# Performance work log

Measured on AMD Instinct MI355X. Metric: run time of the kernel, lower is better.

Reference implementation:

```python
import jax, jax.numpy as jnp
import numpy as np

N = 50000
E = 800000
IN_CH = 128
HID = 128
HEADS = 8
OUT_CH = 40
NEG_SLOPE = 0.2
BN_EPS = 1e-5


def gat_conv(x, src, dst, W, a_src, a_dst, bias, heads, ch, concat):
    # x: [N, F_in]; W: [heads*ch, F_in]; a_src/a_dst: [heads, ch]; bias: [heads*ch] or [ch]
    n = x.shape[0]
    h = (x @ W.T).reshape(n, heads, ch)                      # [N, H, C]
    alpha_src = (h * a_src[None]).sum(-1)                    # [N, H]
    alpha_dst = (h * a_dst[None]).sum(-1)                    # [N, H]
    e = alpha_src[src] + alpha_dst[dst]                      # [E, H]
    e = jax.nn.leaky_relu(e, NEG_SLOPE)
    # segment softmax over incoming edges of each destination node
    emax = jax.ops.segment_max(e, dst, num_segments=n)       # [N, H]
    ee = jnp.exp(e - emax[dst])
    denom = jax.ops.segment_sum(ee, dst, num_segments=n)     # [N, H]
    alpha = ee / (denom[dst] + 1e-16)                        # [E, H]
    msg = h[src] * alpha[:, :, None]                         # [E, H, C]
    out = jax.ops.segment_sum(msg, dst, num_segments=n)      # [N, H, C]
    out = out.reshape(n, heads * ch) if concat else out.mean(axis=1)
    return out + bias


def batch_norm_eval(x, gamma, beta, mean, var):
    return (x - mean) * jax.lax.rsqrt(var + BN_EPS) * gamma + beta


def setup_inputs() -> dict:
    key = jax.random.key(0)
    ks = jax.random.split(key, 16)
    ch = HID // HEADS  # 16
    s = 1.0 / np.sqrt(IN_CH)
    inp = {
        "x": jax.random.normal(ks[0], (N, IN_CH), dtype=jnp.float32),
        "edge_index": jax.random.randint(ks[1], (2, E), 0, N, dtype=jnp.int64),
        # layer 0
        "W0": jax.random.normal(ks[2], (HEADS * ch, IN_CH), jnp.float32) * s,
        "a_src0": jax.random.normal(ks[3], (HEADS, ch), jnp.float32) * 0.1,
        "a_dst0": jax.random.normal(ks[4], (HEADS, ch), jnp.float32) * 0.1,
        "b0": jnp.zeros((HID,), jnp.float32),
        "bn_g0": jnp.ones((HID,), jnp.float32),
        "bn_b0": jnp.zeros((HID,), jnp.float32),
        "bn_m0": jnp.zeros((HID,), jnp.float32),
        "bn_v0": jnp.ones((HID,), jnp.float32),
        # layer 1
        "W1": jax.random.normal(ks[5], (HEADS * ch, HID), jnp.float32) * (1.0 / np.sqrt(HID)),
        "a_src1": jax.random.normal(ks[6], (HEADS, ch), jnp.float32) * 0.1,
        "a_dst1": jax.random.normal(ks[7], (HEADS, ch), jnp.float32) * 0.1,
        "b1": jnp.zeros((HID,), jnp.float32),
        "bn_g1": jnp.ones((HID,), jnp.float32),
        "bn_b1": jnp.zeros((HID,), jnp.float32),
        "bn_m1": jnp.zeros((HID,), jnp.float32),
        "bn_v1": jnp.ones((HID,), jnp.float32),
        # output layer (heads=1, concat=False)
        "W2": jax.random.normal(ks[8], (OUT_CH, HID), jnp.float32) * (1.0 / np.sqrt(HID)),
        "a_src2": jax.random.normal(ks[9], (1, OUT_CH), jnp.float32) * 0.1,
        "a_dst2": jax.random.normal(ks[10], (1, OUT_CH), jnp.float32) * 0.1,
        "b2": jnp.zeros((OUT_CH,), jnp.float32),
    }
    return inp


def reference(x, edge_index, W0, a_src0, a_dst0, b0, bn_g0, bn_b0, bn_m0, bn_v0,
              W1, a_src1, a_dst1, b1, bn_g1, bn_b1, bn_m1, bn_v1,
              W2, a_src2, a_dst2, b2):
    n = x.shape[0]
    # PyG GATConv adds self-loops by default
    loops = jnp.arange(n, dtype=edge_index.dtype)
    src = jnp.concatenate([edge_index[0], loops])
    dst = jnp.concatenate([edge_index[1], loops])
    ch = HID // HEADS

    h = gat_conv(x, src, dst, W0, a_src0, a_dst0, b0, HEADS, ch, True)
    h = batch_norm_eval(h, bn_g0, bn_b0, bn_m0, bn_v0)
    h = jax.nn.elu(h)
    # dropout: eval mode (identity)

    h = gat_conv(h, src, dst, W1, a_src1, a_dst1, b1, HEADS, ch, True)
    h = batch_norm_eval(h, bn_g1, bn_b1, bn_m1, bn_v1)
    h = jax.nn.elu(h)

    out = gat_conv(h, src, dst, W2, a_src2, a_dst2, b2, 1, OUT_CH, False)
    return out
```

## Files before the change

### kernel.cpp

```cpp
#include <hip/hip_runtime.h>
#include <hip/hip_fp16.h>
#include <math.h>

constexpr float NEG_SLOPE = 0.2f;
constexpr float BN_EPS_C = 1e-5f;

using half8 = __attribute__((ext_vector_type(8))) _Float16;
using f32x4 = __attribute__((ext_vector_type(4))) float;


__global__ __launch_bounds__(256)
void bucket_hist_kernel(const int* __restrict__ ei, int* __restrict__ bucket_count,
                        int E, int N) {
    __shared__ int h[256];
    int t = threadIdx.x;
    h[t] = 0;
    __syncthreads();
    int base = blockIdx.x * 4096;
    int ET = E + N;
#pragma unroll
    for (int q = 0; q < 16; ++q) {
        int i = base + q * 256 + t;
        if (i < ET) {
            int d = (i < E) ? ei[E + i] : (i - E);
            atomicAdd(&h[d >> 8], 1);
        }
    }
    __syncthreads();
    if (h[t] > 0) atomicAdd(&bucket_count[t], h[t]);
}

__global__ __launch_bounds__(256)
void bucket_scan_kernel(const int* __restrict__ bucket_count, int* __restrict__ bucket_ptr,
                        int* __restrict__ gcursor, int* __restrict__ row_ptr,
                        int N, int ET) {
    __shared__ int s[256];
    int t = threadIdx.x;
    int c = bucket_count[t];
    s[t] = c;
    __syncthreads();
    for (int off = 1; off < 256; off <<= 1) {
        int v = (t >= off) ? s[t - off] : 0;
        __syncthreads();
        s[t] += v;
        __syncthreads();
    }
    int excl = s[t] - c;
    bucket_ptr[t] = excl;
    gcursor[t] = excl;
    if (t == 255) {
        bucket_ptr[256] = s[255];
        row_ptr[N] = ET;
    }
}

__global__ __launch_bounds__(256)
void bucket_bin_kernel(const int* __restrict__ ei, int* __restrict__ gcursor,
                       int2* __restrict__ tmp, int E, int N) {
    __shared__ int2 bins[4096];
    __shared__ int lcount[256];
    __shared__ int lofs[256];
    __shared__ int lbase[256];
    __shared__ int lcur[256];
    int t = threadIdx.x;
    lcount[t] = 0;
    __syncthreads();
    int base = blockIdx.x * 4096;
    int ET = E + N;
    int2 pr[16];
#pragma unroll
    for (int q = 0; q < 16; ++q) {
        int i = base + q * 256 + t;
        pr[q] = make_int2(-1, -1);
        if (i < ET) {
            int s, d;
            if (i < E) { s = ei[i]; d = ei[E + i]; }
            else       { s = i - E; d = s; }
            pr[q] = make_int2(d, s);
            atomicAdd(&lcount[d >> 8], 1);
        }
    }
    __syncthreads();
    {
        int c = lcount[t];
        lofs[t] = c;
        __syncthreads();
        for (int off = 1; off < 256; off <<= 1) {
            int v = (t >= off) ? lofs[t - off] : 0;
            __syncthreads();
            lofs[t] += v;
            __syncthreads();
        }
        int excl = lofs[t] - c;
        __syncthreads();
        lofs[t] = excl;
        lcur[t] = excl;
        if (c > 0) lbase[t] = atomicAdd(&gcursor[t], c);
    }
    __syncthreads();
#pragma unroll
    for (int q = 0; q < 16; ++q) {
        if (pr[q].x >= 0) {
            int b = pr[q].x >> 8;
            int p = atomicAdd(&lcur[b], 1);
            bins[p] = pr[q];
        }
    }
    __syncthreads();
    int total = min(4096, ET - base);
    for (int p = t; p < total; p += 256) {
        int2 e = bins[p];
        int b = e.x >> 8;
        tmp[lbase[b] + (p - lofs[b])] = e;
    }
}

__global__ __launch_bounds__(256)
void fine_scatter_kernel(const int2* __restrict__ tmp, const int* __restrict__ bucket_ptr,
                         int* __restrict__ row_ptr, int* __restrict__ srcs, int N) {
    __shared__ int hist[256];
    __shared__ int scanb[256];
    __shared__ int cur[256];
    int b = blockIdx.x, t = threadIdx.x;
    int base = bucket_ptr[b];
    int cnt = bucket_ptr[b + 1] - base;
    int n0 = b << 8;
    hist[t] = 0;
    __syncthreads();
    for (int p = t; p < cnt; p += 256)
        atomicAdd(&hist[tmp[base + p].x - n0], 1);
    __syncthreads();
    int c = hist[t];
    scanb[t] = c;
    __syncthreads();
    for (int off = 1; off < 256; off <<= 1) {
        int v = (t >= off) ? scanb[t - off] : 0;
        __syncthreads();
        scanb[t] += v;
        __syncthreads();
    }
    int excl = scanb[t] - c;
    cur[t] = excl;
    if (n0 + t < N) row_ptr[n0 + t] = base + excl;
    __syncthreads();
    for (int p = t; p < cnt; p += 256) {
        int2 e = tmp[base + p];
        int pos = atomicAdd(&cur[e.x - n0], 1);
        srcs[base + pos] = e.y;
    }
}


__global__ __launch_bounds__(512)
void gemm128_mfma_kernel(const float* __restrict__ X, const float* __restrict__ W,
                         const float* __restrict__ a_src, const float* __restrict__ a_dst,
                         __half* __restrict__ hp, float* __restrict__ asrc,
                         float* __restrict__ adst, int N) {
    __shared__ _Float16 Ah[128][136];
    __shared__ _Float16 Bs[128][136];
    const int t = threadIdx.x;
    const int n0 = blockIdx.x * 128;

#pragma unroll
    for (int i = 0; i < 8; ++i) {
        int lin = t + i * 512;
        int r = lin >> 5;
        int m = lin & 31;
        int gn = n0 + r;
        float4 v = make_float4(0.f, 0.f, 0.f, 0.f);
        if (gn < N) v = *reinterpret_cast<const float4*>(&X[(size_t)gn * 128 + 4 * m]);
        __half2 p0 = __floats2half2_rn(v.x, v.y);
        __half2 p1 = __floats2half2_rn(v.z, v.w);
        uint2 u;
        u.x = *reinterpret_cast<unsigned*>(&p0);
        u.y = *reinterpret_cast<unsigned*>(&p1);
        *reinterpret_cast<uint2*>(&Ah[r][4 * m]) = u;
    }
#pragma unroll
    for (int i = 0; i < 8; ++i) {
        int lin = t + i * 512;
        int n = lin >> 5;
        int m = lin & 31;
        float4 v = *reinterpret_cast<const float4*>(&W[(size_t)n * 128 + 4 * m]);
        __half2 p0 = __floats2half2_rn(v.x, v.y);
        __half2 p1 = __floats2half2_rn(v.z, v.w);
        uint2 u;
        u.x = *reinterpret_cast<unsigned*>(&p0);
        u.y = *reinterpret_cast<unsigned*>(&p1);
        *reinterpret_cast<uint2*>(&Bs[n][4 * m]) = u;
    }
    __syncthreads();

    const int l  = t & 63;
    const int w  = t >> 6;
    const int lr = l & 15;
    const int lg = l >> 4;

    f32x4 acc[8];
#pragma unroll
    for (int tt = 0; tt < 8; ++tt) acc[tt] = (f32x4){0.f, 0.f, 0.f, 0.f};

#pragma unroll
    for (int ks = 0; ks < 4; ++ks) {
        half8 a = *reinterpret_cast<const half8*>(&Ah[16 * w + lr][8 * lg + 32 * ks]);
#pragma unroll
        for (int tt = 0; tt < 8; ++tt) {
            half8 b = *reinterpret_cast<const half8*>(&Bs[16 * tt + lr][8 * lg + 32 * ks]);
            acc[tt] = __builtin_amdgcn_mfma_f32_16x16x32_f16(a, b, acc[tt], 0, 0, 0);
        }
    }

    float av[8], bv[8];
#pragma unroll
    for (int tt = 0; tt < 8; ++tt) {
        av[tt] = a_src[16 * tt + lr];
        bv[tt] = a_dst[16 * tt + lr];
    }
#pragma unroll
    for (int reg = 0; reg < 4; ++reg) {
        int gr = n0 + 16 * w + 4 * lg + reg;
        bool ok = gr < N;
        if (ok) {
#pragma unroll
            for (int tt = 0; tt < 8; ++tt)
                hp[(size_t)gr * 128 + 16 * tt + lr] = __float2half(acc[tt][reg]);
        }
#pragma unroll
        for (int tt = 0; tt < 8; ++tt) {
            float p = acc[tt][reg] * av[tt];
            float q = acc[tt][reg] * bv[tt];
#pragma unroll
            for (int off = 1; off < 16; off <<= 1) {
                p += __shfl_xor(p, off, 16);
                q += __shfl_xor(q, off, 16);
            }
            if (ok && lr == tt) {
                asrc[(size_t)gr * 8 + tt] = p;
                adst[(size_t)gr * 8 + tt] = q;
            }
        }
    }
}


__global__ __launch_bounds__(256)
void gemm40_mfma_kernel(const float* __restrict__ X, const float* __restrict__ W,
                        const float* __restrict__ a_src, const float* __restrict__ a_dst,
                        __half* __restrict__ hp, float* __restrict__ asrc,
                        float* __restrict__ adst, int N) {
    __shared__ _Float16 Ah[64][136];
    __shared__ _Float16 Bs[48][136];
    const int t = threadIdx.x;
    const int n0 = blockIdx.x * 64;

#pragma unroll
    for (int i = 0; i < 8; ++i) {
        int lin = t + i * 256;
        int r = lin >> 5;
        int m = lin & 31;
        int gn = n0 + r;
        float4 v = make_float4(0.f, 0.f, 0.f, 0.f);
        if (gn < N) v = *reinterpret_cast<const float4*>(&X[(size_t)gn * 128 + 4 * m]);
        __half2 p0 = __floats2half2_rn(v.x, v.y);
        __half2 p1 = __floats2half2_rn(v.z, v.w);
        uint2 u;
        u.x = *reinterpret_cast<unsigned*>(&p0);
        u.y = *reinterpret_cast<unsigned*>(&p1);
        *reinterpret_cast<uint2*>(&Ah[r][4 * m]) = u;
    }
#pragma unroll
    for (int i = 0; i < 6; ++i) {
        int lin = t + i * 256;
        if (lin < 1536) {
            int n = lin >> 5;
            int m = lin & 31;
            float4 v = make_float4(0.f, 0.f, 0.f, 0.f);
            if (n < 40) v = *reinterpret_cast<const float4*>(&W[(size_t)n * 128 + 4 * m]);
            __half2 p0 = __floats2half2_rn(v.x, v.y);
            __half2 p1 = __floats2half2_rn(v.z, v.w);
            uint2 u;
            u.x = *reinterpret_cast<unsigned*>(&p0);
            u.y = *reinterpret_cast<unsigned*>(&p1);
            *reinterpret_cast<uint2*>(&Bs[n][4 * m]) = u;
        }
    }
    __syncthreads();

    const int l  = t & 63;
    const int w  = t >> 6;
    const int lr = l & 15;
    const int lg = l >> 4;

    f32x4 acc[3];
#pragma unroll
    for (int tt = 0; tt < 3; ++tt) acc[tt] = (f32x4){0.f, 0.f, 0.f, 0.f};

#pragma unroll
    for (int ks = 0; ks < 4; ++ks) {
        half8 a = *reinterpret_cast<const half8*>(&Ah[16 * w + lr][8 * lg + 32 * ks]);
#pragma unroll
        for (int tt = 0; tt < 3; ++tt) {
            half8 b = *reinterpret_cast<const half8*>(&Bs[16 * tt + lr][8 * lg + 32 * ks]);
            acc[tt] = __builtin_amdgcn_mfma_f32_16x16x32_f16(a, b, acc[tt], 0, 0, 0);
        }
    }

    float av[3], bv[3];
#pragma unroll
    for (int tt = 0; tt < 3; ++tt) {
        int j = 16 * tt + lr;
        av[tt] = (j < 40) ? a_src[j] : 0.f;
        bv[tt] = (j < 40) ? a_dst[j] : 0.f;
    }
#pragma unroll
    for (int reg = 0; reg < 4; ++reg) {
        int gr = n0 + 16 * w + 4 * lg + reg;
        bool ok = gr < N;
        float p = 0.f, q = 0.f;
#pragma unroll
        for (int tt = 0; tt < 3; ++tt) {
            int j = 16 * tt + lr;
            if (ok && j < 40) hp[(size_t)gr * 40 + j] = __float2half(acc[tt][reg]);
            p += acc[tt][reg] * av[tt];
            q += acc[tt][reg] * bv[tt];
        }
#pragma unroll
        for (int off = 1; off < 16; off <<= 1) {
            p += __shfl_xor(p, off, 16);
            q += __shfl_xor(q, off, 16);
        }
        if (ok && lr == 0) {
            asrc[gr] = p;
            adst[gr] = q;
        }
    }
}


__global__ __launch_bounds__(256)
void message128_kernel(const uint4* __restrict__ hh4, const int* __restrict__ row_ptr,
                       const int* __restrict__ srcs,
                       const float* __restrict__ asrc, const float* __restrict__ adst,
                       const float* __restrict__ bias,
                       const float* __restrict__ bn_g, const float* __restrict__ bn_b,
                       const float* __restrict__ bn_m, const float* __restrict__ bn_v,
                       float* __restrict__ out, int N) {
    int node = blockIdx.x * 8 + (threadIdx.x >> 5);
    if (node >= N) return;
    int tc = threadIdx.x & 31;
    int half_id = tc >> 4;
    int cl = tc & 15;
    int hd = cl >> 1;
    int beg = row_ptr[node], end = row_ptr[node + 1];
    float ad = adst[(size_t)node * 8 + hd];
    float ssum = 0.f;
    float acc[8];
#pragma unroll
    for (int q = 0; q < 8; ++q) acc[q] = 0.f;

    int j = beg;
    for (; j + 2 <= end; j += 2) {
        int s = srcs[j + half_id];
        uint4 u = hh4[(size_t)s * 16 + cl];
        float e = asrc[(size_t)s * 8 + hd] + ad;
        e = (e > 0.f) ? e : NEG_SLOPE * e;
        float wgt = __expf(e);
        ssum += wgt;
        float2 f0 = __half22float2(*reinterpret_cast<const __half2*>(&u.x));
        float2 f1 = __half22float2(*reinterpret_cast<const __half2*>(&u.y));
        float2 f2 = __half22float2(*reinterpret_cast<const __half2*>(&u.z));
        float2 f3 = __half22float2(*reinterpret_cast<const __half2*>(&u.w));
        acc[0] += wgt * f0.x; acc[1] += wgt * f0.y;
        acc[2] += wgt * f1.x; acc[3] += wgt * f1.y;
        acc[4] += wgt * f2.x; acc[5] += wgt * f2.y;
        acc[6] += wgt * f3.x; acc[7] += wgt * f3.y;
    }
    if (j < end && half_id == 0) {
        int s = srcs[j];
        uint4 u = hh4[(size_t)s * 16 + cl];
        float e = asrc[(size_t)s * 8 + hd] + ad;
        e = (e > 0.f) ? e : NEG_SLOPE * e;
        float wgt = __expf(e);
        ssum += wgt;
        float2 f0 = __half22float2(*reinterpret_cast<const __half2*>(&u.x));
        float2 f1 = __half22float2(*reinterpret_cast<const __half2*>(&u.y));
        float2 f2 = __half22float2(*reinterpret_cast<const __half2*>(&u.z));
        float2 f3 = __half22float2(*reinterpret_cast<const __half2*>(&u.w));
        acc[0] += wgt * f0.x; acc[1] += wgt * f0.y;
        acc[2] += wgt * f1.x; acc[3] += wgt * f1.y;
        acc[4] += wgt * f2.x; acc[5] += wgt * f2.y;
        acc[6] += wgt * f3.x; acc[7] += wgt * f3.y;
    }
    ssum += __shfl_xor(ssum, 16);
#pragma unroll
    for (int q = 0; q < 8; ++q) acc[q] += __shfl_xor(acc[q], 16);

    if (half_id == 0) {
        float inv = 1.0f / (ssum + 1e-16f);
        int c = cl * 8;
        float r[8];
#pragma unroll
        for (int pp = 0; pp < 2; ++pp) {
            int cc = c + 4 * pp;
            float4 bi = *reinterpret_cast<const float4*>(&bias[cc]);
            float4 g  = *reinterpret_cast<const float4*>(&bn_g[cc]);
            float4 bb = *reinterpret_cast<const float4*>(&bn_b[cc]);
            float4 mm = *reinterpret_cast<const float4*>(&bn_m[cc]);
            float4 vv = *reinterpret_cast<const float4*>(&bn_v[cc]);
            r[4 * pp + 0] = (acc[4 * pp + 0] * inv + bi.x - mm.x) * rsqrtf(vv.x + BN_EPS_C) * g.x + bb.x;
            r[4 * pp + 1] = (acc[4 * pp + 1] * inv + bi.y - mm.y) * rsqrtf(vv.y + BN_EPS_C) * g.y + bb.y;
            r[4 * pp + 2] = (acc[4 * pp + 2] * inv + bi.z - mm.z) * rsqrtf(vv.z + BN_EPS_C) * g.z + bb.z;
            r[4 * pp + 3] = (acc[4 * pp + 3] * inv + bi.w - mm.w) * rsqrtf(vv.w + BN_EPS_C) * g.w + bb.w;
        }
#pragma unroll
        for (int q = 0; q < 8; ++q) r[q] = (r[q] > 0.f) ? r[q] : expm1f(r[q]);
        *reinterpret_cast<float4*>(&out[(size_t)node * 128 + c]) =
            make_float4(r[0], r[1], r[2], r[3]);
        *reinterpret_cast<float4*>(&out[(size_t)node * 128 + c + 4]) =
            make_float4(r[4], r[5], r[6], r[7]);
    }
}


__global__ __launch_bounds__(256)
void message40_kernel(const uint2* __restrict__ hh2, const int* __restrict__ row_ptr,
                      const int* __restrict__ srcs,
                      const float* __restrict__ asrc, const float* __restrict__ adst,
                      const float* __restrict__ b2, float* __restrict__ out, int N) {
    int node = blockIdx.x * 16 + (threadIdx.x >> 4);
    if (node >= N) return;
    int tc = threadIdx.x & 15;
    int beg = row_ptr[node], end = row_ptr[node + 1];
    float ad = adst[node];
    float ssum = 0.f;
    float4 acc = make_float4(0.f, 0.f, 0.f, 0.f);
    int j = beg;
    for (; j + 2 <= end; j += 2) {
        int s0 = srcs[j];
        int s1 = srcs[j + 1];
        uint2 u0 = make_uint2(0u, 0u), u1 = make_uint2(0u, 0u);
        if (tc < 10) {
            u0 = hh2[(size_t)s0 * 10 + tc];
            u1 = hh2[(size_t)s1 * 10 + tc];
        }
        float e0 = asrc[s0] + ad;
        float e1 = asrc[s1] + ad;
        e0 = (e0 > 0.f) ? e0 : NEG_SLOPE * e0;
        e1 = (e1 > 0.f) ? e1 : NEG_SLOPE * e1;
        float w0 = __expf(e0);
        float w1 = __expf(e1);
        ssum += w0 + w1;
        float2 a0 = __half22float2(*reinterpret_cast<const __half2*>(&u0.x));
        float2 b0 = __half22float2(*reinterpret_cast<const __half2*>(&u0.y));
        float2 a1 = __half22float2(*reinterpret_cast<const __half2*>(&u1.x));
        float2 b1 = __half22float2(*reinterpret_cast<const __half2*>(&u1.y));
        acc.x += w0 * a0.x + w1 * a1.x;
        acc.y += w0 * a0.y + w1 * a1.y;
        acc.z += w0 * b0.x + w1 * b1.x;
        acc.w += w0 * b0.y + w1 * b1.y;
    }
    if (j < end) {
        int s0 = srcs[j];
        uint2 u0 = make_uint2(0u, 0u);
        if (tc < 10) u0 = hh2[(size_t)s0 * 10 + tc];
        float e0 = asrc[s0] + ad;
        e0 = (e0 > 0.f) ? e0 : NEG_SLOPE * e0;
        float w0 = __expf(e0);
        ssum += w0;
        float2 a0 = __half22float2(*reinterpret_cast<const __half2*>(&u0.x));
        float2 b0 = __half22float2(*reinterpret_cast<const __half2*>(&u0.y));
        acc.x += w0 * a0.x;
        acc.y += w0 * a0.y;
        acc.z += w0 * b0.x;
        acc.w += w0 * b0.y;
    }
    if (tc < 10) {
        float inv = 1.0f / (ssum + 1e-16f);
        int c = tc * 4;
        float4 bi = *reinterpret_cast<const float4*>(&b2[c]);
        *reinterpret_cast<float4*>(&out[(size_t)node * 40 + c]) =
            make_float4(acc.x * inv + bi.x, acc.y * inv + bi.y,
                        acc.z * inv + bi.z, acc.w * inv + bi.w);
    }
}


static inline char* align256(char* p) {
    return (char*)(((uintptr_t)p + 255) & ~(uintptr_t)255);
}

extern "C" void kernel_launch(void* const* d_in, const int* in_sizes, int n_in,
                              void* d_out, int out_size, void* d_ws, size_t ws_size,
                              hipStream_t stream) {
    const float* x   = (const float*)d_in[0];
    const int*   ei  = (const int*)d_in[1];
    const float* W0  = (const float*)d_in[2];
    const float* as0 = (const float*)d_in[3];
    const float* ad0 = (const float*)d_in[4];
    const float* b0  = (const float*)d_in[5];
    const float* g0  = (const float*)d_in[6];
    const float* bb0 = (const float*)d_in[7];
    const float* m0  = (const float*)d_in[8];
    const float* v0  = (const float*)d_in[9];
    const float* W1  = (const float*)d_in[10];
    const float* as1 = (const float*)d_in[11];
    const float* ad1 = (const float*)d_in[12];
    const float* b1  = (const float*)d_in[13];
    const float* g1  = (const float*)d_in[14];
    const float* bb1 = (const float*)d_in[15];
    const float* m1  = (const float*)d_in[16];
    const float* v1  = (const float*)d_in[17];
    const float* W2  = (const float*)d_in[18];
    const float* as2 = (const float*)d_in[19];
    const float* ad2 = (const float*)d_in[20];
    const float* b2  = (const float*)d_in[21];

    const int N  = in_sizes[0] / 128;
    const int E  = in_sizes[1] / 2;
    const int ET = E + N;
    const int NBUK = (N + 255) >> 8;
    const int NEB  = (ET + 4095) / 4096;

    char* wsp = (char*)d_ws;
    int* bucket_count = (int*)wsp;  wsp = align256(wsp + 256 * 4);
    int* bucket_ptr   = (int*)wsp;  wsp = align256(wsp + 257 * 4);
    int* gcursor      = (int*)wsp;  wsp = align256(wsp + 256 * 4);
    int* row_ptr      = (int*)wsp;  wsp = align256(wsp + (size_t)(N + 1) * 4);
    int2* tmp         = (int2*)wsp; wsp = align256(wsp + (size_t)ET * 8);
    int* srcs         = (int*)wsp;  wsp = align256(wsp + (size_t)ET * 4);
    __half* hh        = (__half*)wsp; wsp = align256(wsp + (size_t)N * 128 * 2);
    __half* h2        = (__half*)wsp; wsp = align256(wsp + (size_t)N * 40 * 2);
    float* feat       = (float*)wsp;  wsp = align256(wsp + (size_t)N * 128 * 4);
    float* asr        = (float*)wsp;  wsp = align256(wsp + (size_t)N * 8 * 4);
    float* adt        = (float*)wsp;  wsp = align256(wsp + (size_t)N * 8 * 4);

    hipMemsetAsync(bucket_count, 0, 256 * 4, stream);
    bucket_hist_kernel<<<NEB, 256, 0, stream>>>(ei, bucket_count, E, N);
    bucket_scan_kernel<<<1, 256, 0, stream>>>(bucket_count, bucket_ptr, gcursor, row_ptr, N, ET);
    bucket_bin_kernel<<<NEB, 256, 0, stream>>>(ei, gcursor, tmp, E, N);
    fine_scatter_kernel<<<NBUK, 256, 0, stream>>>(tmp, bucket_ptr, row_ptr, srcs, N);

    const int g128 = (N + 127) / 128;
    const int g40  = (N + 63) / 64;

    gemm128_mfma_kernel<<<g128, 512, 0, stream>>>(x, W0, as0, ad0, hh, asr, adt, N);
    message128_kernel<<<(N + 7) / 8, 256, 0, stream>>>((const uint4*)hh, row_ptr, srcs, asr, adt,
                                                       b0, g0, bb0, m0, v0, feat, N);
    gemm128_mfma_kernel<<<g128, 512, 0, stream>>>(feat, W1, as1, ad1, hh, asr, adt, N);
    message128_kernel<<<(N + 7) / 8, 256, 0, stream>>>((const uint4*)hh, row_ptr, srcs, asr, adt,
                                                       b1, g1, bb1, m1, v1, feat, N);
    gemm40_mfma_kernel<<<g40, 256, 0, stream>>>(feat, W2, as2, ad2, h2, asr, adt, N);
    message40_kernel<<<(N + 15) / 16, 256, 0, stream>>>((const uint2*)h2, row_ptr, srcs,
                                                        asr, adt, b2, (float*)d_out, N);
}
```

Before: 225.1 us.

## Store intermediate features in fp16, pre-convert weights, drop LDS staging in GEMMs

The message kernels now write the post-BN/ELU features as fp16 instead of fp32, which halves the feature write and the next GEMM's read. A new small kernel converts the weight matrices to fp16 once per call. The GEMM kernels drop shared-memory staging and read A and B fragments straight from global memory, with a smaller 64-row tile. The 128-wide message kernel also gains a 4-edge unrolled loop for more memory-level parallelism. This costs an extra launch and uncoalesced direct B loads, and adds fp16 rounding on intermediate activations.

After: 236.7 us. 1.05x slower.

```diff
diff --git a/kernel.cpp b/kernel.cpp
--- a/kernel.cpp
+++ b/kernel.cpp
@@ -7,6 +7,19 @@
 
 using half8 = __attribute__((ext_vector_type(8))) _Float16;
 using f32x4 = __attribute__((ext_vector_type(4))) float;
+
+
+__global__ void cvt_w_kernel(const float* __restrict__ W0, const float* __restrict__ W1,
+                             const float* __restrict__ W2,
+                             __half* __restrict__ W0h, __half* __restrict__ W1h,
+                             __half* __restrict__ W2h) {
+    int i = blockIdx.x * blockDim.x + threadIdx.x;
+    if (i < 16384) {
+        W0h[i] = __float2half(W0[i]);
+        W1h[i] = __float2half(W1[i]);
+    }
+    if (i < 6144) W2h[i] = __float2half(i < 5120 ? W2[i] : 0.f);
+}
 
 
 __global__ __launch_bounds__(256)
@@ -151,50 +164,20 @@
 }
 
 
-__global__ __launch_bounds__(512)
-void gemm128_mfma_kernel(const float* __restrict__ X, const float* __restrict__ W,
+template<bool AHALF>
+__global__ __launch_bounds__(256)
+void gemm128_mfma_kernel(const void* __restrict__ Xv, const __half* __restrict__ W16,
                          const float* __restrict__ a_src, const float* __restrict__ a_dst,
                          __half* __restrict__ hp, float* __restrict__ asrc,
                          float* __restrict__ adst, int N) {
-    __shared__ _Float16 Ah[128][136];
-    __shared__ _Float16 Bs[128][136];
     const int t = threadIdx.x;
-    const int n0 = blockIdx.x * 128;
-
-#pragma unroll
-    for (int i = 0; i < 8; ++i) {
-        int lin = t + i * 512;
-        int r = lin >> 5;
-        int m = lin & 31;
-        int gn = n0 + r;
-        float4 v = make_float4(0.f, 0.f, 0.f, 0.f);
-        if (gn < N) v = *reinterpret_cast<const float4*>(&X[(size_t)gn * 128 + 4 * m]);
-        __half2 p0 = __floats2half2_rn(v.x, v.y);
-        __half2 p1 = __floats2half2_rn(v.z, v.w);
-        uint2 u;
-        u.x = *reinterpret_cast<unsigned*>(&p0);
-        u.y = *reinterpret_cast<unsigned*>(&p1);
-        *reinterpret_cast<uint2*>(&Ah[r][4 * m]) = u;
-    }
-#pragma unroll
-    for (int i = 0; i < 8; ++i) {
-        int lin = t + i * 512;
-        int n = lin >> 5;
-        int m = lin & 31;
-        float4 v = *reinterpret_cast<const float4*>(&W[(size_t)n * 128 + 4 * m]);
-        __half2 p0 = __floats2half2_rn(v.x, v.y);
-        __half2 p1 = __floats2half2_rn(v.z, v.w);
-        uint2 u;
-        u.x = *reinterpret_cast<unsigned*>(&p0);
-        u.y = *reinterpret_cast<unsigned*>(&p1);
-        *reinterpret_cast<uint2*>(&Bs[n][4 * m]) = u;
-    }
-    __syncthreads();
-
     const int l  = t & 63;
     const int w  = t >> 6;
     const int lr = l & 15;
     const int lg = l >> 4;
+    const int n0 = blockIdx.x * 64;
+    const int rowA = n0 + 16 * w + lr;
+    const bool rokA = rowA < N;
 
     f32x4 acc[8];
 #pragma unroll
@@ -202,10 +185,29 @@
 
 #pragma unroll
     for (int ks = 0; ks < 4; ++ks) {
-        half8 a = *reinterpret_cast<const half8*>(&Ah[16 * w + lr][8 * lg + 32 * ks]);
+        half8 a;
+        if (rokA) {
+            if constexpr (AHALF) {
+                const __half* X = (const __half*)Xv;
+                a = *reinterpret_cast<const half8*>(&X[(size_t)rowA * 128 + 8 * lg + 32 * ks]);
+            } else {
+                const float* X = (const float*)Xv;
+                const float* p = &X[(size_t)rowA * 128 + 8 * lg + 32 * ks];
+                float4 v0 = *reinterpret_cast<const float4*>(p);
+                float4 v1 = *reinterpret_cast<const float4*>(p + 4);
+                a[0] = (_Float16)v0.x; a[1] = (_Float16)v0.y;
+                a[2] = (_Float16)v0.z; a[3] = (_Float16)v0.w;
+                a[4] = (_Float16)v1.x; a[5] = (_Float16)v1.y;
+                a[6] = (_Float16)v1.z; a[7] = (_Float16)v1.w;
+            }
+        } else {
+#pragma unroll
+            for (int q = 0; q < 8; ++q) a[q] = (_Float16)0.f;
+        }
 #pragma unroll
         for (int tt = 0; tt < 8; ++tt) {
-            half8 b = *reinterpret_cast<const half8*>(&Bs[16 * tt + lr][8 * lg + 32 * ks]);
+            half8 b = *reinterpret_cast<const half8*>(
+                &W16[(size_t)(16 * tt + lr) * 128 + 8 * lg + 32 * ks]);
             acc[tt] = __builtin_amdgcn_mfma_f32_16x16x32_f16(a, b, acc[tt], 0, 0, 0);
         }
     }
@@ -244,52 +246,18 @@
 
 
 __global__ __launch_bounds__(256)
-void gemm40_mfma_kernel(const float* __restrict__ X, const float* __restrict__ W,
+void gemm40_mfma_kernel(const __half* __restrict__ X, const __half* __restrict__ W16,
                         const float* __restrict__ a_src, const float* __restrict__ a_dst,
                         __half* __restrict__ hp, float* __restrict__ asrc,
                         float* __restrict__ adst, int N) {
-    __shared__ _Float16 Ah[64][136];
-    __shared__ _Float16 Bs[48][136];
     const int t = threadIdx.x;
-    const int n0 = blockIdx.x * 64;
-
-#pragma unroll
-    for (int i = 0; i < 8; ++i) {
-        int lin = t + i * 256;
-        int r = lin >> 5;
-        int m = lin & 31;
-        int gn = n0 + r;
-        float4 v = make_float4(0.f, 0.f, 0.f, 0.f);
-        if (gn < N) v = *reinterpret_cast<const float4*>(&X[(size_t)gn * 128 + 4 * m]);
-        __half2 p0 = __floats2half2_rn(v.x, v.y);
-        __half2 p1 = __floats2half2_rn(v.z, v.w);
-        uint2 u;
-        u.x = *reinterpret_cast<unsigned*>(&p0);
-        u.y = *reinterpret_cast<unsigned*>(&p1);
-        *reinterpret_cast<uint2*>(&Ah[r][4 * m]) = u;
-    }
-#pragma unroll
-    for (int i = 0; i < 6; ++i) {
-        int lin = t + i * 256;
-        if (lin < 1536) {
-            int n = lin >> 5;
-            int m = lin & 31;
-            float4 v = make_float4(0.f, 0.f, 0.f, 0.f);
-            if (n < 40) v = *reinterpret_cast<const float4*>(&W[(size_t)n * 128 + 4 * m]);
-            __half2 p0 = __floats2half2_rn(v.x, v.y);
-            __half2 p1 = __floats2half2_rn(v.z, v.w);
-            uint2 u;
-            u.x = *reinterpret_cast<unsigned*>(&p0);
-            u.y = *reinterpret_cast<unsigned*>(&p1);
-            *reinterpret_cast<uint2*>(&Bs[n][4 * m]) = u;
-        }
-    }
-    __syncthreads();
-
     const int l  = t & 63;
     const int w  = t >> 6;
     const int lr = l & 15;
     const int lg = l >> 4;
+    const int n0 = blockIdx.x * 64;
+    const int rowA = n0 + 16 * w + lr;
+    const bool rokA = rowA < N;
 
     f32x4 acc[3];
 #pragma unroll
@@ -297,10 +265,17 @@
 
 #pragma unroll
     for (int ks = 0; ks < 4; ++ks) {
-        half8 a = *reinterpret_cast<const half8*>(&Ah[16 * w + lr][8 * lg + 32 * ks]);
+        half8 a;
+        if (rokA) {
+            a = *reinterpret_cast<const half8*>(&X[(size_t)rowA * 128 + 8 * lg + 32 * ks]);
+        } else {
+#pragma unroll
+            for (int q = 0; q < 8; ++q) a[q] = (_Float16)0.f;
+        }
 #pragma unroll
         for (int tt = 0; tt < 3; ++tt) {
-            half8 b = *reinterpret_cast<const half8*>(&Bs[16 * tt + lr][8 * lg + 32 * ks]);
+            half8 b = *reinterpret_cast<const half8*>(
+                &W16[(size_t)(16 * tt + lr) * 128 + 8 * lg + 32 * ks]);
             acc[tt] = __builtin_amdgcn_mfma_f32_16x16x32_f16(a, b, acc[tt], 0, 0, 0);
         }
     }
@@ -344,7 +319,7 @@
                        const float* __restrict__ bias,
                        const float* __restrict__ bn_g, const float* __restrict__ bn_b,
                        const float* __restrict__ bn_m, const float* __restrict__ bn_v,
-                       float* __restrict__ out, int N) {
+                       __half* __restrict__ out16, int N) {
     int node = blockIdx.x * 8 + (threadIdx.x >> 5);
     if (node >= N) return;
     int tc = threadIdx.x & 31;
@@ -359,6 +334,31 @@
     for (int q = 0; q < 8; ++q) acc[q] = 0.f;
 
     int j = beg;
+    for (; j + 4 <= end; j += 4) {
+        int sA = srcs[j + half_id];
+        int sB = srcs[j + 2 + half_id];
+        uint4 uA = hh4[(size_t)sA * 16 + cl];
+        uint4 uB = hh4[(size_t)sB * 16 + cl];
+        float eA = asrc[(size_t)sA * 8 + hd] + ad;
+        float eB = asrc[(size_t)sB * 8 + hd] + ad;
+        eA = (eA > 0.f) ? eA : NEG_SLOPE * eA;
+        eB = (eB > 0.f) ? eB : NEG_SLOPE * eB;
+        float wA = __expf(eA);
+        float wB = __expf(eB);
+        ssum += wA + wB;
+        float2 a0 = __half22float2(*reinterpret_cast<const __half2*>(&uA.x));
+        float2 a1 = __half22float2(*reinterpret_cast<const __half2*>(&uA.y));
+        float2 a2 = __half22float2(*reinterpret_cast<const __half2*>(&uA.z));
+        float2 a3 = __half22float2(*reinterpret_cast<const __half2*>(&uA.w));
+        float2 b0 = __half22float2(*reinterpret_cast<const __half2*>(&uB.x));
+        float2 b1 = __half22float2(*reinterpret_cast<const __half2*>(&uB.y));
+        float2 b2 = __half22float2(*reinterpret_cast<const __half2*>(&uB.z));
+        float2 b3 = __half22float2(*reinterpret_cast<const __half2*>(&uB.w));
+        acc[0] += wA * a0.x + wB * b0.x; acc[1] += wA * a0.y + wB * b0.y;
+        acc[2] += wA * a1.x + wB * b1.x; acc[3] += wA * a1.y + wB * b1.y;
+        acc[4] += wA * a2.x + wB * b2.x; acc[5] += wA * a2.y + wB * b2.y;
+        acc[6] += wA * a3.x + wB * b3.x; acc[7] += wA * a3.y + wB * b3.y;
+    }
     for (; j + 2 <= end; j += 2) {
         int s = srcs[j + half_id];
         uint4 u = hh4[(size_t)s * 16 + cl];
@@ -412,12 +412,13 @@
             r[4 * pp + 2] = (acc[4 * pp + 2] * inv + bi.z - mm.z) * rsqrtf(vv.z + BN_EPS_C) * g.z + bb.z;
             r[4 * pp + 3] = (acc[4 * pp + 3] * inv + bi.w - mm.w) * rsqrtf(vv.w + BN_EPS_C) * g.w + bb.w;
         }
-#pragma unroll
-        for (int q = 0; q < 8; ++q) r[q] = (r[q] > 0.f) ? r[q] : expm1f(r[q]);
-        *reinterpret_cast<float4*>(&out[(size_t)node * 128 + c]) =
-            make_float4(r[0], r[1], r[2], r[3]);
-        *reinterpret_cast<float4*>(&out[(size_t)node * 128 + c + 4]) =
-            make_float4(r[4], r[5], r[6], r[7]);
+        half8 o;
+#pragma unroll
+        for (int q = 0; q < 8; ++q) {
+            float rv = (r[q] > 0.f) ? r[q] : expm1f(r[q]);
+            o[q] = (_Float16)rv;
+        }
+        *reinterpret_cast<half8*>(&out16[(size_t)node * 128 + c]) = o;
     }
 }
 
@@ -530,9 +531,14 @@
     int* srcs         = (int*)wsp;  wsp = align256(wsp + (size_t)ET * 4);
     __half* hh        = (__half*)wsp; wsp = align256(wsp + (size_t)N * 128 * 2);
     __half* h2        = (__half*)wsp; wsp = align256(wsp + (size_t)N * 40 * 2);
-    float* feat       = (float*)wsp;  wsp = align256(wsp + (size_t)N * 128 * 4);
+    __half* feat      = (__half*)wsp; wsp = align256(wsp + (size_t)N * 128 * 2);
     float* asr        = (float*)wsp;  wsp = align256(wsp + (size_t)N * 8 * 4);
     float* adt        = (float*)wsp;  wsp = align256(wsp + (size_t)N * 8 * 4);
+    __half* W0h       = (__half*)wsp; wsp = align256(wsp + 16384 * 2);
+    __half* W1h       = (__half*)wsp; wsp = align256(wsp + 16384 * 2);
+    __half* W2h       = (__half*)wsp; wsp = align256(wsp + 6144 * 2);
+
+    cvt_w_kernel<<<64, 256, 0, stream>>>(W0, W1, W2, W0h, W1h, W2h);
 
     hipMemsetAsync(bucket_count, 0, 256 * 4, stream);
     bucket_hist_kernel<<<NEB, 256, 0, stream>>>(ei, bucket_count, E, N);
@@ -540,16 +546,15 @@
     bucket_bin_kernel<<<NEB, 256, 0, stream>>>(ei, gcursor, tmp, E, N);
     fine_scatter_kernel<<<NBUK, 256, 0, stream>>>(tmp, bucket_ptr, row_ptr, srcs, N);
 
-    const int g128 = (N + 127) / 128;
-    const int g40  = (N + 63) / 64;
-
-    gemm128_mfma_kernel<<<g128, 512, 0, stream>>>(x, W0, as0, ad0, hh, asr, adt, N);
+    const int g64 = (N + 63) / 64;
+
+    gemm128_mfma_kernel<false><<<g64, 256, 0, stream>>>(x, W0h, as0, ad0, hh, asr, adt, N);
     message128_kernel<<<(N + 7) / 8, 256, 0, stream>>>((const uint4*)hh, row_ptr, srcs, asr, adt,
                                                        b0, g0, bb0, m0, v0, feat, N);
-    gemm128_mfma_kernel<<<g128, 512, 0, stream>>>(feat, W1, as1, ad1, hh, asr, adt, N);
+    gemm128_mfma_kernel<true><<<g64, 256, 0, stream>>>(feat, W1h, as1, ad1, hh, asr, adt, N);
     message128_kernel<<<(N + 7) / 8, 256, 0, stream>>>((const uint4*)hh, row_ptr, srcs, asr, adt,
                                                        b1, g1, bb1, m1, v1, feat, N);
-    gemm40_mfma_kernel<<<g40, 256, 0, stream>>>(feat, W2, as2, ad2, h2, asr, adt, N);
+    gemm40_mfma_kernel<<<g64, 256, 0, stream>>>(feat, W2h, as2, ad2, h2, asr, adt, N);
     message40_kernel<<<(N + 15) / 16, 256, 0, stream>>>((const uint2*)h2, row_ptr, srcs,
                                                         asr, adt, b2, (float*)d_out, N);
 }
```
